# Kernel tuning notes

Measured on AMD Instinct MI355X. Metric: run time of the kernel, lower is better.

## Reference

```python
import jax, jax.numpy as jnp
import numpy as np

B, N, D_IN, H, F = 2, 2048, 512, 8, 64
NEG_SLOPE = 0.2


def setup_inputs() -> dict:
    key = jax.random.key(0)
    k0, k1, k2, k3 = jax.random.split(key, 4)
    nodes = jax.random.normal(k0, (B, N, D_IN), dtype=jnp.float32)
    edges = jax.random.randint(k1, (B, N, N, 1), 0, 2).astype(jnp.int32)
    # ensure every node has at least one neighbor (self-loop) so softmax is finite
    idx = jnp.arange(N)
    edges = edges.at[:, idx, idx, :].set(1)
    W = jax.random.normal(k2, (D_IN, H * F), dtype=jnp.float32) * 0.02
    a = jax.random.normal(k3, (2 * F,), dtype=jnp.float32) * 0.02
    return {"nodes": nodes, "edges": edges, "W": W, "a": a}


def reference(nodes, edges, W, a):
    b, n, _ = nodes.shape
    mapped = (nodes @ W).reshape(b, n, H, F)  # [B,N,H,F]
    # additive attention: attn([m_i ; m_j]) = a_l . m_i + a_r . m_j
    a_l, a_r = a[:F], a[F:]
    el = jnp.einsum('bnhf,f->bnh', mapped, a_l)
    er = jnp.einsum('bnhf,f->bnh', mapped, a_r)
    scores = jax.nn.leaky_relu(el[:, :, None, :] + er[:, None, :, :], negative_slope=NEG_SLOPE)  # [B,N,N,H]
    mask = edges != 0  # [B,N,N,1] broadcasts over heads
    scores = jnp.where(mask, scores, -jnp.inf)
    attn_weights = jax.nn.softmax(scores, axis=2)  # softmax over neighbors j
    attn_res = jnp.einsum('bijh,bjhf->bihf', attn_weights, mapped)  # [B,N,H,F]
    # is_concat=False path: mean over heads, then sigmoid
    return jax.nn.sigmoid(attn_res.mean(axis=2))  # [B,N,F]
```

## Files before the change

### kernel.cpp

```cpp
#include <hip/hip_runtime.h>
#include <hip/hip_bf16.h>
#include <math.h>

#define Bq   2
#define Nq   2048
#define DIN  512
#define Hq   8
#define Fq   64
#define NEG  0.2f

using short8 = __attribute__((ext_vector_type(8))) short;
using f32x4  = __attribute__((ext_vector_type(4))) float;

__device__ inline unsigned int bf16_rne(float x) {
    unsigned int u = __float_as_uint(x);
    u += 0x7fffu + ((u >> 16) & 1u);
    return u >> 16;
}

#define AFRAG_BLOCKS 256
#define WFRAG_BLOCKS 128

__global__ __launch_bounds__(256) void prep_kernel(
    const float* __restrict__ nodes, ushort* __restrict__ Afrag,
    const float* __restrict__ W,     ushort* __restrict__ Wfrag)
{
    __shared__ __align__(16) char smem[16 * 516 * 4];
    const int bid = blockIdx.x;
    const int t   = threadIdx.x;

    if (bid < AFRAG_BLOCKS) {
        float (*As)[516] = (float(*)[516])smem;
        const int mt = bid;
        {
            const int row = t >> 4, c = t & 15;
#pragma unroll
            for (int i = 0; i < 8; i++) {
                float4 v = *(const float4*)&nodes[((size_t)mt * 16 + row) * DIN + (c + i * 16) * 4];
                *(float4*)&As[row][(c + i * 16) * 4] = v;
            }
        }
        __syncthreads();
        const int lane = t & 63, ksg = t >> 6;
        const int quad = lane >> 4, l15 = lane & 15;
#pragma unroll
        for (int k2 = 0; k2 < 4; k2++) {
            int ks = ksg * 4 + k2;
            const float* src = &As[l15][ks * 32 + quad * 8];
            float4 f0 = *(const float4*)src;
            float4 f1 = *(const float4*)(src + 4);
            uint4 pk;
            pk.x = bf16_rne(f0.x) | (bf16_rne(f0.y) << 16);
            pk.y = bf16_rne(f0.z) | (bf16_rne(f0.w) << 16);
            pk.z = bf16_rne(f1.x) | (bf16_rne(f1.y) << 16);
            pk.w = bf16_rne(f1.z) | (bf16_rne(f1.w) << 16);
            *(uint4*)(Afrag + ((size_t)(mt * 16 + ks) * 64 + lane) * 8) = pk;
        }
        return;
    }

    {
        float (*Ws)[68] = (float(*)[68])smem;
        const int id = bid - AFRAG_BLOCKS;
        const int ks = id & 15, h = id >> 4;
        {
            const int row = t >> 3, c = t & 7;
            const float* src = &W[(size_t)(ks * 32 + row) * (Hq * Fq) + h * 64 + c * 8];
            float4 v0 = *(const float4*)src;
            float4 v1 = *(const float4*)(src + 4);
            *(float4*)&Ws[row][c * 8]     = v0;
            *(float4*)&Ws[row][c * 8 + 4] = v1;
        }
        __syncthreads();
        const int lane = t & 63, nf = t >> 6;
        const int quad = lane >> 4, l15 = lane & 15;
        float f[8];
#pragma unroll
        for (int jj = 0; jj < 8; jj++) f[jj] = Ws[quad * 8 + jj][nf * 16 + l15];
        uint4 pk;
        pk.x = bf16_rne(f[0]) | (bf16_rne(f[1]) << 16);
        pk.y = bf16_rne(f[2]) | (bf16_rne(f[3]) << 16);
        pk.z = bf16_rne(f[4]) | (bf16_rne(f[5]) << 16);
        pk.w = bf16_rne(f[6]) | (bf16_rne(f[7]) << 16);
        *(uint4*)(Wfrag + (((size_t)(h * 16 + ks) * 4 + nf) * 64 + lane) * 8) = pk;
    }
}

#define GEMM_BLOCKS 512
#define PACK_BLOCKS 1024

__global__ __launch_bounds__(256) void work_kernel(
    const ushort* __restrict__ Afrag, const ushort* __restrict__ Wfrag,
    const float*  __restrict__ avec,
    ushort* __restrict__ Vfrag,
    float* __restrict__ el_t,
    float* __restrict__ er_t,
    const int* __restrict__ edges, unsigned int* __restrict__ ebT)
{
    const int bid = blockIdx.x;
    const int t   = threadIdx.x;

    if (bid >= GEMM_BLOCKS) {
        int gid = (bid - GEMM_BLOCKS) * 256 + t;
        int i = gid & 2047;
        int w = (gid >> 11) & 63;
        int b = gid >> 17;
        const int4* ep = (const int4*)(edges + (((size_t)b * Nq + i) * Nq + w * 32));
        unsigned int word = 0;
#pragma unroll
        for (int c = 0; c < 8; c++) {
            int4 v = ep[c];
            word |= (v.x != 0 ? 1u : 0u) << (c * 4);
            word |= (v.y != 0 ? 1u : 0u) << (c * 4 + 1);
            word |= (v.z != 0 ? 1u : 0u) << (c * 4 + 2);
            word |= (v.w != 0 ? 1u : 0u) << (c * 4 + 3);
        }
        ebT[((size_t)b * 64 + w) * Nq + i] = word;
        return;
    }

    const int lane = t & 63;
    const int wv   = t >> 6;
    const int quad = lane >> 4;
    const int l15  = lane & 15;
    const int h    = bid >> 6;
    const int mt   = (bid & 63) * 4 + wv;
    const int row0 = mt * 16;

    const ushort* ap = Afrag + (size_t)mt * 8192 + lane * 8;
    const ushort* bp = Wfrag + (size_t)h * 32768 + lane * 8;

    f32x4 zero4 = {0.f, 0.f, 0.f, 0.f};
    f32x4 acc[4] = {zero4, zero4, zero4, zero4};

    short8 a0, a1, b0[4], b1[4];
    a0 = *(const short8*)(ap);
#pragma unroll
    for (int nf = 0; nf < 4; nf++) b0[nf] = *(const short8*)(bp + nf * 512);

    for (int ks = 0; ks < 16; ks += 2) {
        a1 = *(const short8*)(ap + (ks + 1) * 512);
#pragma unroll
        for (int nf = 0; nf < 4; nf++) b1[nf] = *(const short8*)(bp + (ks + 1) * 2048 + nf * 512);
#pragma unroll
        for (int nf = 0; nf < 4; nf++)
            acc[nf] = __builtin_amdgcn_mfma_f32_16x16x32_bf16(a0, b0[nf], acc[nf], 0, 0, 0);
        a0 = *(const short8*)(ap + (ks + 2) * 512);
#pragma unroll
        for (int nf = 0; nf < 4; nf++) b0[nf] = *(const short8*)(bp + (ks + 2) * 2048 + nf * 512);
#pragma unroll
        for (int nf = 0; nf < 4; nf++)
            acc[nf] = __builtin_amdgcn_mfma_f32_16x16x32_bf16(a1, b1[nf], acc[nf], 0, 0, 0);
    }

    float aL[4], aR[4];
#pragma unroll
    for (int nf = 0; nf < 4; nf++) {
        aL[nf] = avec[nf * 16 + l15];
        aR[nf] = avec[Fq + nf * 16 + l15];
    }
    const int bb = row0 >> 11;
    const int bh = bb * Hq + h;
#pragma unroll
    for (int r = 0; r < 4; r++) {
        float pl = acc[0][r] * aL[0] + acc[1][r] * aL[1] + acc[2][r] * aL[2] + acc[3][r] * aL[3];
        float pr = acc[0][r] * aR[0] + acc[1][r] * aR[1] + acc[2][r] * aR[2] + acc[3][r] * aR[3];
#pragma unroll
        for (int off = 1; off < 16; off <<= 1) {
            pl += __shfl_xor(pl, off, 64);
            pr += __shfl_xor(pr, off, 64);
        }
        if (l15 == 0) {
            int n = (row0 + quad * 4 + r) & (Nq - 1);
            el_t[(size_t)bh * Nq + n] = pl;
            er_t[(size_t)bh * Nq + n] = pr;
        }
    }

    const int n_base = row0 & (Nq - 1);
    const int sblk   = n_base >> 5;
    const int quadp  = ((wv & 1) << 1) | (quad >> 1);
    const int jj0    = (quad & 1) * 4;
#pragma unroll
    for (int nf = 0; nf < 4; nf++) {
        unsigned int r0 = bf16_rne(acc[nf][0]), r1 = bf16_rne(acc[nf][1]);
        unsigned int r2 = bf16_rne(acc[nf][2]), r3 = bf16_rne(acc[nf][3]);
        uint2 pk;
        pk.x = r0 | (r1 << 16);
        pk.y = r2 | (r3 << 16);
        size_t off = ((((size_t)bh * 64 + sblk) * 4 + nf) * 64 + quadp * 16 + l15) * 8 + jj0;
        *(uint2*)(Vfrag + off) = pk;
    }
}

__global__ __launch_bounds__(512, 4) void attn_kernel(
    const float* __restrict__ el_t, const float* __restrict__ er_t,
    const ushort* __restrict__ Vfrag,
    const unsigned int* __restrict__ ebT, float* __restrict__ attn)
{
    const int lane = threadIdx.x & 63;
    const int wv8  = threadIdx.x >> 6;
    const int rg   = wv8 & 3;
    const int kh   = wv8 >> 2;
    const int quad = lane >> 4;
    const int l15  = lane & 15;
    const int bid  = blockIdx.x;
    const int it   = bid & 31;
    const int h    = (bid >> 5) & 7;
    const int b    = bid >> 8;
    const int bh   = b * Hq + h;
    const int i0   = it * 64 + rg * 16;

    __shared__ float smax[8];
    const float* errow = er_t + (size_t)bh * Nq;
    float mx = -INFINITY;
#pragma unroll
    for (int ii = 0; ii < 4; ii++) mx = fmaxf(mx, errow[threadIdx.x + ii * 512]);
#pragma unroll
    for (int off = 32; off > 0; off >>= 1) mx = fmaxf(mx, __shfl_xor(mx, off, 64));
    if (lane == 0) smax[wv8] = mx;
    __syncthreads();
    float emax = smax[0];
#pragma unroll
    for (int q = 1; q < 8; q++) emax = fmaxf(emax, smax[q]);

    const float elv = el_t[(size_t)bh * Nq + i0 + l15];
    const float xm  = elv + emax;
    const float m0  = fmaxf(xm, NEG * xm);
    const float R   = 1.4426950408889634f;
    const float R2  = NEG * R;
    const float c1  = (elv - m0) * R, c2 = (NEG * elv - m0) * R;

    const float*        erp = er_t + (size_t)bh * Nq;
    const ushort*       vp  = Vfrag + (size_t)bh * 131072 + lane * 8;
    const unsigned int* e0p = ebT + (size_t)b * 64 * Nq + i0 + l15;

    f32x4 zero4 = {0.f, 0.f, 0.f, 0.f};
    f32x4 acc[4] = {zero4, zero4, zero4, zero4};
    float l0 = 0.f;

    const int s_beg = kh * 32, s_end = kh * 32 + 32;
    for (int s = s_beg; s < s_end; s++) {
        short8 vb0 = *(const short8*)(vp + s * 2048);
        short8 vb1 = *(const short8*)(vp + s * 2048 + 512);
        short8 vb2 = *(const short8*)(vp + s * 2048 + 1024);
        short8 vb3 = *(const short8*)(vp + s * 2048 + 1536);
        unsigned int w0 = e0p[(size_t)s * Nq];
        float4 ea  = *(const float4*)(erp + s * 32 + quad * 8);
        float4 ebv = *(const float4*)(erp + s * 32 + quad * 8 + 4);

        const unsigned int wq0 = w0 >> (quad * 8);
        float er8[8] = {ea.x, ea.y, ea.z, ea.w, ebv.x, ebv.y, ebv.z, ebv.w};
        unsigned int u0[8];
#pragma unroll
        for (int jj = 0; jj < 8; jj++) {
            float e  = er8[jj];
            float t0 = fmaxf(fmaf(R, e, c1), fmaf(R2, e, c2));
            float x0 = __builtin_amdgcn_exp2f(t0);
            int k0 = ((int)(wq0 << (31 - jj))) >> 31;
            u0[jj] = __float_as_uint(x0) & (unsigned int)k0;
            l0 += __uint_as_float(u0[jj]);
        }
        union { short8 s8; unsigned int w[4]; } af0;
        af0.w[0] = __builtin_amdgcn_perm(u0[1], u0[0], 0x07060302);
        af0.w[1] = __builtin_amdgcn_perm(u0[3], u0[2], 0x07060302);
        af0.w[2] = __builtin_amdgcn_perm(u0[5], u0[4], 0x07060302);
        af0.w[3] = __builtin_amdgcn_perm(u0[7], u0[6], 0x07060302);

        acc[0] = __builtin_amdgcn_mfma_f32_16x16x32_bf16(af0.s8, vb0, acc[0], 0, 0, 0);
        acc[1] = __builtin_amdgcn_mfma_f32_16x16x32_bf16(af0.s8, vb1, acc[1], 0, 0, 0);
        acc[2] = __builtin_amdgcn_mfma_f32_16x16x32_bf16(af0.s8, vb2, acc[2], 0, 0, 0);
        acc[3] = __builtin_amdgcn_mfma_f32_16x16x32_bf16(af0.s8, vb3, acc[3], 0, 0, 0);
    }

    __shared__ __align__(16) float lds_acc[4][16][65];
    __shared__ float lds_l[4][64];
    if (kh == 1) {
#pragma unroll
        for (int nf = 0; nf < 4; nf++)
#pragma unroll
            for (int r = 0; r < 4; r++)
                lds_acc[rg][quad * 4 + r][nf * 16 + l15] = acc[nf][r];
        lds_l[rg][lane] = l0;
    }
    __syncthreads();
    if (kh == 0) {
#pragma unroll
        for (int nf = 0; nf < 4; nf++)
#pragma unroll
            for (int r = 0; r < 4; r++)
                acc[nf][r] += lds_acc[rg][quad * 4 + r][nf * 16 + l15];
        l0 += lds_l[rg][lane];
        l0 += __shfl_xor(l0, 16, 64);
        l0 += __shfl_xor(l0, 32, 64);
        float lr[4];
#pragma unroll
        for (int r = 0; r < 4; r++) lr[r] = __shfl(l0, quad * 4 + r, 64);

#pragma unroll
        for (int nf = 0; nf < 4; nf++)
#pragma unroll
            for (int r = 0; r < 4; r++)
                attn[(((size_t)b * Nq + i0 + quad * 4 + r) * Hq + h) * Fq + nf * 16 + l15] =
                    acc[nf][r] / lr[r];
    }
}

__global__ __launch_bounds__(256) void out_kernel(
    const float* __restrict__ attn, float* __restrict__ out)
{
    const int idx = blockIdx.x * 256 + threadIdx.x;
    const int f   = idx & 63;
    const int bn  = idx >> 6;
    const float* p = attn + (size_t)bn * Hq * Fq + f;
    float s = 0.f;
#pragma unroll
    for (int h = 0; h < Hq; h++) s += p[h * Fq];
    s *= (1.f / Hq);
    out[idx] = 1.f / (1.f + __expf(-s));
}

extern "C" void kernel_launch(void* const* d_in, const int* in_sizes, int n_in,
                              void* d_out, int out_size, void* d_ws, size_t ws_size,
                              hipStream_t stream) {
    const float* nodes = (const float*)d_in[0];
    const int*   edges = (const int*)d_in[1];
    const float* W     = (const float*)d_in[2];
    const float* a     = (const float*)d_in[3];
    float* out = (float*)d_out;

    char* ws = (char*)d_ws;
    ushort* Afrag = (ushort*)ws;           ws += (size_t)Bq * Nq * DIN * 2;
    ushort* Wfrag = (ushort*)ws;           ws += (size_t)DIN * Hq * Fq * 2;
    ushort* Vfrag = (ushort*)ws;           ws += (size_t)Bq * Hq * Nq * Fq * 2;
    float*  el_t  = (float*)ws;            ws += (size_t)Bq * Hq * Nq * 4;
    float*  er_t  = (float*)ws;            ws += (size_t)Bq * Hq * Nq * 4;
    unsigned int* ebT = (unsigned int*)ws; ws += (size_t)Bq * (Nq / 32) * Nq * 4;
    float*  attn  = (float*)ws;

    prep_kernel<<<AFRAG_BLOCKS + WFRAG_BLOCKS, 256, 0, stream>>>(nodes, Afrag, W, Wfrag);
    work_kernel<<<GEMM_BLOCKS + PACK_BLOCKS, 256, 0, stream>>>(
        Afrag, Wfrag, a, Vfrag, el_t, er_t, edges, ebT);
    attn_kernel<<<Bq * Hq * (Nq / 64), 512, 0, stream>>>(el_t, er_t, Vfrag, ebT, attn);
    out_kernel<<<(Bq * Nq * Fq) / 256, 256, 0, stream>>>(attn, out);
}
```

Measured before the change: 125.8 us.

## Factor leaky-relu exponent into precomputed per-node exp terms, drop max pass

Rewrites exp(leaky_relu(el+er)) as max(exp(er), exp(-0.8*el)*exp(0.2*er)), with a common factor exp(el) that cancels in the softmax. The two per-node exponentials are computed once in the GEMM epilogue, so the attention inner loop swaps eight exp2 calls for one multiply and one max each. The per-block max-reduction prologue and its __syncthreads are removed. In exchange it loads two float arrays per step instead of one, and it gives up max-subtraction, which risks overflow or underflow for large scores. That risk is small here given the scale of the weights.

Measured after the change: 132.0 us. +4.9%, slower.

```diff
diff --git a/kernel.cpp b/kernel.cpp
--- a/kernel.cpp
+++ b/kernel.cpp
@@ -94,7 +94,8 @@
     const float*  __restrict__ avec,
     ushort* __restrict__ Vfrag,
     float* __restrict__ el_t,
-    float* __restrict__ er_t,
+    float* __restrict__ f1_t,
+    float* __restrict__ f2_t,
     const int* __restrict__ edges, unsigned int* __restrict__ ebT)
 {
     const int bid = blockIdx.x;
@@ -161,6 +162,7 @@
     }
     const int bb = row0 >> 11;
     const int bh = bb * Hq + h;
+    const float R = 1.4426950408889634f;
 #pragma unroll
     for (int r = 0; r < 4; r++) {
         float pl = acc[0][r] * aL[0] + acc[1][r] * aL[1] + acc[2][r] * aL[2] + acc[3][r] * aL[3];
@@ -173,7 +175,8 @@
         if (l15 == 0) {
             int n = (row0 + quad * 4 + r) & (Nq - 1);
             el_t[(size_t)bh * Nq + n] = pl;
-            er_t[(size_t)bh * Nq + n] = pr;
+            f1_t[(size_t)bh * Nq + n] = __builtin_amdgcn_exp2f(R * pr);
+            f2_t[(size_t)bh * Nq + n] = __builtin_amdgcn_exp2f(NEG * R * pr);
         }
     }
 
@@ -194,8 +197,8 @@
 }
 
 __global__ __launch_bounds__(512, 4) void attn_kernel(
-    const float* __restrict__ el_t, const float* __restrict__ er_t,
-    const ushort* __restrict__ Vfrag,
+    const float* __restrict__ el_t, const float* __restrict__ f1_t,
+    const float* __restrict__ f2_t, const ushort* __restrict__ Vfrag,
     const unsigned int* __restrict__ ebT, float* __restrict__ attn)
 {
     const int lane = threadIdx.x & 63;
@@ -211,27 +214,12 @@
     const int bh   = b * Hq + h;
     const int i0   = it * 64 + rg * 16;
 
-    __shared__ float smax[8];
-    const float* errow = er_t + (size_t)bh * Nq;
-    float mx = -INFINITY;
-#pragma unroll
-    for (int ii = 0; ii < 4; ii++) mx = fmaxf(mx, errow[threadIdx.x + ii * 512]);
-#pragma unroll
-    for (int off = 32; off > 0; off >>= 1) mx = fmaxf(mx, __shfl_xor(mx, off, 64));
-    if (lane == 0) smax[wv8] = mx;
-    __syncthreads();
-    float emax = smax[0];
-#pragma unroll
-    for (int q = 1; q < 8; q++) emax = fmaxf(emax, smax[q]);
-
-    const float elv = el_t[(size_t)bh * Nq + i0 + l15];
-    const float xm  = elv + emax;
-    const float m0  = fmaxf(xm, NEG * xm);
-    const float R   = 1.4426950408889634f;
-    const float R2  = NEG * R;
-    const float c1  = (elv - m0) * R, c2 = (NEG * elv - m0) * R;
-
-    const float*        erp = er_t + (size_t)bh * Nq;
+    const float R    = 1.4426950408889634f;
+    const float elv  = el_t[(size_t)bh * Nq + i0 + l15];
+    const float rrat = __builtin_amdgcn_exp2f(-0.8f * R * elv);
+
+    const float*        f1p = f1_t + (size_t)bh * Nq;
+    const float*        f2p = f2_t + (size_t)bh * Nq;
     const ushort*       vp  = Vfrag + (size_t)bh * 131072 + lane * 8;
     const unsigned int* e0p = ebT + (size_t)b * 64 * Nq + i0 + l15;
 
@@ -246,19 +234,20 @@
         short8 vb2 = *(const short8*)(vp + s * 2048 + 1024);
         short8 vb3 = *(const short8*)(vp + s * 2048 + 1536);
         unsigned int w0 = e0p[(size_t)s * Nq];
-        float4 ea  = *(const float4*)(erp + s * 32 + quad * 8);
-        float4 ebv = *(const float4*)(erp + s * 32 + quad * 8 + 4);
+        float4 fa  = *(const float4*)(f1p + s * 32 + quad * 8);
+        float4 fab = *(const float4*)(f1p + s * 32 + quad * 8 + 4);
+        float4 fb  = *(const float4*)(f2p + s * 32 + quad * 8);
+        float4 fbb = *(const float4*)(f2p + s * 32 + quad * 8 + 4);
 
         const unsigned int wq0 = w0 >> (quad * 8);
-        float er8[8] = {ea.x, ea.y, ea.z, ea.w, ebv.x, ebv.y, ebv.z, ebv.w};
+        float f1v[8] = {fa.x, fa.y, fa.z, fa.w, fab.x, fab.y, fab.z, fab.w};
+        float f2v[8] = {fb.x, fb.y, fb.z, fb.w, fbb.x, fbb.y, fbb.z, fbb.w};
         unsigned int u0[8];
 #pragma unroll
         for (int jj = 0; jj < 8; jj++) {
-            float e  = er8[jj];
-            float t0 = fmaxf(fmaf(R, e, c1), fmaf(R2, e, c2));
-            float x0 = __builtin_amdgcn_exp2f(t0);
+            float g = fmaxf(f1v[jj], rrat * f2v[jj]);
             int k0 = ((int)(wq0 << (31 - jj))) >> 31;
-            u0[jj] = __float_as_uint(x0) & (unsigned int)k0;
+            u0[jj] = __float_as_uint(g) & (unsigned int)k0;
             l0 += __uint_as_float(u0[jj]);
         }
         union { short8 s8; unsigned int w[4]; } af0;
@@ -334,13 +323,14 @@
     ushort* Wfrag = (ushort*)ws;           ws += (size_t)DIN * Hq * Fq * 2;
     ushort* Vfrag = (ushort*)ws;           ws += (size_t)Bq * Hq * Nq * Fq * 2;
     float*  el_t  = (float*)ws;            ws += (size_t)Bq * Hq * Nq * 4;
-    float*  er_t  = (float*)ws;            ws += (size_t)Bq * Hq * Nq * 4;
+    float*  f1_t  = (float*)ws;            ws += (size_t)Bq * Hq * Nq * 4;
+    float*  f2_t  = (float*)ws;            ws += (size_t)Bq * Hq * Nq * 4;
     unsigned int* ebT = (unsigned int*)ws; ws += (size_t)Bq * (Nq / 32) * Nq * 4;
     float*  attn  = (float*)ws;
 
     prep_kernel<<<AFRAG_BLOCKS + WFRAG_BLOCKS, 256, 0, stream>>>(nodes, Afrag, W, Wfrag);
     work_kernel<<<GEMM_BLOCKS + PACK_BLOCKS, 256, 0, stream>>>(
-        Afrag, Wfrag, a, Vfrag, el_t, er_t, edges, ebT);
-    attn_kernel<<<Bq * Hq * (Nq / 64), 512, 0, stream>>>(el_t, er_t, Vfrag, ebT, attn);
+        Afrag, Wfrag, a, Vfrag, el_t, f1_t, f2_t, edges, ebT);
+    attn_kernel<<<Bq * Hq * (Nq / 64), 512, 0, stream>>>(el_t, f1_t, f2_t, Vfrag, ebT, attn);
     out_kernel<<<(Bq * Nq * Fq) / 256, 256, 0, stream>>>(attn, out);
 }
```
